# Performance work log

Measured on AMD Instinct MI355X. Metric: run time of the kernel, lower is better.

The kernel has to match this reference:

```python
import jax, jax.numpy as jnp
import numpy as np

EMBED = 4096
NUM_Q = 32
NUM_KV = 8
GROUPS = NUM_Q // NUM_KV  # 4
HEAD_DIM = EMBED // NUM_Q  # 128
KV_DIM = HEAD_DIM * NUM_KV  # 1024


def setup_inputs() -> dict:
    key = jax.random.key(0)
    ks = jax.random.split(key, 12)
    B, S = 2, 2048
    s = 0.02
    return {
        "query": jax.random.normal(ks[0], (B, S, EMBED), jnp.float32),
        "key": jax.random.normal(ks[1], (B, S, EMBED), jnp.float32),
        "value": jax.random.normal(ks[2], (B, S, EMBED), jnp.float32),
        # weights stored [in, out] (i.e. torch weight transposed)
        "Wq": jax.random.normal(ks[3], (EMBED, EMBED), jnp.float32) * s,
        "bq": jnp.zeros((EMBED,), jnp.float32),
        "Wk": jax.random.normal(ks[4], (EMBED, KV_DIM), jnp.float32) * s,
        "bk": jnp.zeros((KV_DIM,), jnp.float32),
        "Wv": jax.random.normal(ks[5], (EMBED, KV_DIM), jnp.float32) * s,
        "bv": jnp.zeros((KV_DIM,), jnp.float32),
        "Wo": jax.random.normal(ks[6], (EMBED, EMBED), jnp.float32) * s,
        "bo": jnp.zeros((EMBED,), jnp.float32),
    }


def reference(query, key, value, Wq, bq, Wk, bk, Wv, bv, Wo, bo):
    B, S, _ = query.shape
    Q = query @ Wq + bq                      # [B,S,E]
    K = key @ Wk + bk                        # [B,S,KV_DIM]
    V = value @ Wv + bv                      # [B,S,KV_DIM]
    # Q head h attends kv head h // GROUPS (repeat_interleave semantics):
    # reshape Q heads as (kv_head, group)
    Q = Q.reshape(B, S, NUM_KV, GROUPS, HEAD_DIM).transpose(0, 2, 3, 1, 4)  # [B,Hkv,G,S,D]
    K = K.reshape(B, S, NUM_KV, HEAD_DIM).transpose(0, 2, 1, 3)             # [B,Hkv,S,D]
    V = V.reshape(B, S, NUM_KV, HEAD_DIM).transpose(0, 2, 1, 3)             # [B,Hkv,S,D]
    scale = 1.0 / jnp.sqrt(jnp.asarray(HEAD_DIM, query.dtype))
    scores = jnp.einsum('bhgqd,bhkd->bhgqk', Q, K) * scale  # [B,Hkv,G,S,S]
    w = jax.nn.softmax(scores, axis=-1)
    y = jnp.einsum('bhgqk,bhkd->bhgqd', w, V)                # [B,Hkv,G,S,D]
    # back to [B,S,E] with head order (kv_head*GROUPS + group)
    y = y.transpose(0, 3, 1, 2, 4).reshape(B, S, EMBED)
    return y @ Wo + bo  # dropout is identity in eval mode
```

## Files before the change

kernel.cpp:

```cpp
#include <hip/hip_runtime.h>

typedef unsigned short u16;
typedef __attribute__((ext_vector_type(8))) short s16x8;
typedef __attribute__((ext_vector_type(4))) short s16x4;
typedef __attribute__((ext_vector_type(4))) float f32x4;

#define DEVI static __device__ __forceinline__

constexpr int BATCH = 2;
constexpr int SEQ   = 2048;
constexpr int EMB   = 4096;
constexpr int NQ    = 32;
constexpr int NKV   = 8;
constexpr int HD    = 128;
constexpr int KVD   = 1024;
constexpr int MR    = BATCH * SEQ;

constexpr float SCL = 0.08838834764831845f * 1.4426950408889634f;


DEVI u16 f2bf(float f) {
  union { float f; unsigned u; } x; x.f = f;
  unsigned r = x.u + 0x7FFFu + ((x.u >> 16) & 1u);
  return (u16)(r >> 16);
}

DEVI void mfma_acc(f32x4& c, s16x8 a, s16x8 b) {
  asm volatile("v_mfma_f32_16x16x32_bf16 %0, %1, %2, %0" : "+v"(c) : "v"(a), "v"(b));
}

DEVI void gload16(const void* g, void* l) {
  __builtin_amdgcn_global_load_lds(
      (const __attribute__((address_space(1))) void*)g,
      (__attribute__((address_space(3))) void*)l, 16, 0, 0);
}

DEVI float fexp2(float x) {
#if __has_builtin(__builtin_amdgcn_exp2f)
  return __builtin_amdgcn_exp2f(x);
#else
  return exp2f(x);
#endif
}

DEVI void store_out(u16* C, size_t idx, float v)   { C[idx] = f2bf(v); }
DEVI void store_out(float* C, size_t idx, float v) { C[idx] = v; }


__global__ __launch_bounds__(256) void prep(
    const float* __restrict__ q_in, const float* __restrict__ k_in,
    const float* __restrict__ v_in,
    u16* __restrict__ qb, u16* __restrict__ kb, u16* __restrict__ vb,
    const float* __restrict__ Wq, const float* __restrict__ Wo,
    const float* __restrict__ Wk, const float* __restrict__ Wv,
    u16* __restrict__ Tq, u16* __restrict__ To,
    u16* __restrict__ Tk, u16* __restrict__ Tv) {
  __shared__ u16 tile[32][33];
  const int tid = threadIdx.x;
  int id = blockIdx.x;

  if (id < 24576) {
    const int tn = id >> 13;
    const float* in = (tn == 0) ? q_in : (tn == 1) ? k_in : v_in;
    u16* out = (tn == 0) ? qb : (tn == 1) ? kb : vb;
    const size_t i = (size_t)(id & 8191) * 256 + tid;
    const float4* p4 = (const float4*)in;
    float4 x = p4[2 * i], y = p4[2 * i + 1];
    u16 t[8];
    t[0] = f2bf(x.x); t[1] = f2bf(x.y); t[2] = f2bf(x.z); t[3] = f2bf(x.w);
    t[4] = f2bf(y.x); t[5] = f2bf(y.y); t[6] = f2bf(y.z); t[7] = f2bf(y.w);
    *(s16x8*)(out + 8 * i) = *(const s16x8*)t;
    return;
  }

  id -= 24576;
  int z, rem;
  if (id < 16384)      { z = 0; rem = id; }
  else if (id < 32768) { z = 1; rem = id - 16384; }
  else if (id < 36864) { z = 2; rem = id - 32768; }
  else                 { z = 3; rem = id - 36864; }
  const int nt = (z < 2) ? 128 : 32;
  const int Nd = (z < 2) ? EMB : KVD;
  const int bx = rem % nt, by = rem / nt;
  const float* W = (z == 0) ? Wq : (z == 1) ? Wo : (z == 2) ? Wk : Wv;
  u16* Wt = (z == 0) ? Tq : (z == 1) ? To : (z == 2) ? Tk : Tv;
  const float s = (z == 0) ? SCL : 1.0f;
  const int tx = tid & 31, ty = tid >> 5;
  const int n0 = bx * 32, k0 = by * 32;
#pragma unroll
  for (int j = 0; j < 4; ++j)
    tile[ty + 8 * j][tx] = f2bf(W[(size_t)(k0 + ty + 8 * j) * Nd + n0 + tx] * s);
  __syncthreads();
#pragma unroll
  for (int j = 0; j < 4; ++j)
    Wt[(size_t)(n0 + ty + 8 * j) * EMB + k0 + tx] = tile[tx][ty + 8 * j];
}


template <typename OT, int MODE>
DEVI void gemm_body(const u16* __restrict__ A, const u16* __restrict__ Bt,
                    const float* __restrict__ bias, float bscl, OT* __restrict__ C,
                    int M, int N, int K, int m0, int n0,
                    u16* As, u16* Bs) {
  const int tid = threadIdx.x;
  const int lane = tid & 63, w = tid >> 6;
  const int wr = w >> 1, wc = w & 1;
  const int l15 = lane & 15, g = lane >> 4;
  const int srow = lane >> 3;
  const int schunk = lane & 7;

  f32x4 acc[4][4] = {};

  const u16* Ag = A  + (size_t)(m0 + w * 8 + srow) * K + ((schunk ^ srow) << 3);
  const u16* Bg = Bt + (size_t)(n0 + w * 8 + srow) * K + ((schunk ^ srow) << 3);
  u16* Al = As + w * 512;
  u16* Bl = Bs + w * 512;

  for (int k0 = 0; k0 < K; k0 += 64) {
    __syncthreads();
#pragma unroll
    for (int p = 0; p < 4; ++p) {
      gload16(Ag + (size_t)(p * 32) * K + k0, Al + p * 2048);
      gload16(Bg + (size_t)(p * 32) * K + k0, Bl + p * 2048);
    }
    __syncthreads();

#pragma unroll
    for (int ks = 0; ks < 2; ++ks) {
      s16x8 af[4], bfr[4];
#pragma unroll
      for (int rt = 0; rt < 4; ++rt) {
        const int blk = ((ks << 2) | g) ^ (l15 & 7);
        af[rt] = *(const s16x8*)(As + (wr * 64 + rt * 16 + l15) * 64 + (blk << 3));
      }
#pragma unroll
      for (int ct = 0; ct < 4; ++ct) {
        const int blk = ((ks << 2) | g) ^ (l15 & 7);
        bfr[ct] = *(const s16x8*)(Bs + (wc * 64 + ct * 16 + l15) * 64 + (blk << 3));
      }
#pragma unroll
      for (int rt = 0; rt < 4; ++rt)
#pragma unroll
        for (int ct = 0; ct < 4; ++ct)
          mfma_acc(acc[rt][ct], af[rt], bfr[ct]);
    }
  }

#pragma unroll
  for (int ct = 0; ct < 4; ++ct) {
    const int col = n0 + wc * 64 + ct * 16 + l15;
    const float bv = bias[col] * bscl;
#pragma unroll
    for (int rt = 0; rt < 4; ++rt) {
      const int row0 = m0 + wr * 64 + rt * 16 + g * 4;
      if constexpr (MODE == 0) {
#pragma unroll
        for (int i = 0; i < 4; ++i)
          store_out(C, (size_t)(row0 + i) * N + col, acc[rt][ct][i] + bv);
      } else {
        const int b = row0 >> 11, s0 = row0 & 2047;
        const int h = col >> 7, d = col & 127;
        u16 t4[4];
#pragma unroll
        for (int i = 0; i < 4; ++i) t4[i] = f2bf(acc[rt][ct][i] + bv);
        *(s16x4*)((u16*)C + ((size_t)(b * NKV + h) * HD + d) * SEQ + s0) =
            *(const s16x4*)t4;
      }
    }
  }
}

__global__ __launch_bounds__(256) void gemm_o(const u16* __restrict__ A,
                                              const u16* __restrict__ Bt,
                                              const float* __restrict__ bias,
                                              float* __restrict__ C) {
  __shared__ __align__(16) u16 As[128 * 64];
  __shared__ __align__(16) u16 Bs[128 * 64];
  const int d = blockIdx.x + blockIdx.y * 32;
  const int t = (d & 7) * 128 + (d >> 3);
  const int x = t >> 5, y = t & 31;
  gemm_body<float, 0>(A, Bt, bias, 1.0f, C, MR, EMB, EMB, y * 128, x * 128, As, Bs);
}

__global__ __launch_bounds__(256) void gemm_proj(
    const u16* __restrict__ qb, const u16* __restrict__ kb, const u16* __restrict__ vb,
    const u16* __restrict__ Wqt, const u16* __restrict__ Wkt, const u16* __restrict__ Wvt,
    const float* __restrict__ bq, const float* __restrict__ bk, const float* __restrict__ bv,
    u16* __restrict__ Qp, u16* __restrict__ Kpp, u16* __restrict__ Vtt) {
  __shared__ __align__(16) u16 As[128 * 64];
  __shared__ __align__(16) u16 Bs[128 * 64];
  const int d = blockIdx.x + blockIdx.y * 48;
  const int t = (d & 7) * 192 + (d >> 3);
  const int x = t >> 5, y = t & 31;
  if (x < 32)
    gemm_body<u16, 0>(qb, Wqt, bq, SCL, Qp, MR, EMB, EMB, y * 128, x * 128, As, Bs);
  else if (x < 40)
    gemm_body<u16, 0>(kb, Wkt, bk, 1.0f, Kpp, MR, KVD, EMB, y * 128, (x - 32) * 128, As, Bs);
  else
    gemm_body<u16, 1>(vb, Wvt, bv, 1.0f, Vtt, MR, KVD, EMB, y * 128, (x - 40) * 128, As, Bs);
}


__global__ __launch_bounds__(256, 2) void attn(const u16* __restrict__ Q,
                                               const u16* __restrict__ Kp,
                                               const u16* __restrict__ Vt,
                                               u16* __restrict__ Y) {
  __shared__ __align__(16) u16 Kb[2][64 * 128];
  __shared__ __align__(16) u16 Vb[2][128 * 64];

  const int tid = threadIdx.x, lane = tid & 63, w = tid >> 6;
  const int l15 = lane & 15, g = lane >> 4;
  const int d_ = blockIdx.x;
  const int t_ = (d_ & 7) * 128 + (d_ >> 3);
  const int bz = t_ >> 4, b = bz >> 5, qh = bz & 31, h = qh >> 2;
  const int q0 = (t_ & 15) * 128;

  s16x8 qf[2][4];
  const u16* qptr = Q + (size_t)(b * SEQ + q0 + w * 32) * EMB + qh * HD;
#pragma unroll
  for (int rt = 0; rt < 2; ++rt)
#pragma unroll
    for (int ks = 0; ks < 4; ++ks)
      qf[rt][ks] = *(const s16x8*)(qptr + (size_t)(rt * 16 + l15) * EMB + ks * 32 + g * 8);

  const u16* kbase = Kp + (size_t)b * SEQ * KVD + h * HD;
  const u16* vbase = Vt + (size_t)(b * NKV + h) * HD * SEQ;

  auto stage = [&](int buf, int kv0) {
#pragma unroll
    for (int p = 0; p < 4; ++p) {
      int r = p * 16 + w * 4 + (lane >> 4);
      const u16* src = kbase + (size_t)(kv0 + r) * KVD + (((lane & 15) ^ (r & 7)) << 3);
      gload16(src, &Kb[buf][p * 2048 + w * 512]);
    }
#pragma unroll
    for (int p = 0; p < 4; ++p) {
      int r = p * 32 + w * 8 + (lane >> 3);
      const u16* src = vbase + (size_t)r * SEQ + kv0 + (((lane & 7) ^ (r & 7)) << 3);
      gload16(src, &Vb[buf][p * 2048 + w * 512]);
    }
  };

  f32x4 o[2][8] = {};
  float m_[2] = {-1e30f, -1e30f}, l_[2] = {0.f, 0.f};

  stage(0, 0);
  __syncthreads();

  for (int t = 0; t < SEQ / 64; ++t) {
    const int cur = t & 1;
    if (t < SEQ / 64 - 1) stage(cur ^ 1, (t + 1) * 64);

    f32x4 sacc[2][4] = {};
    __builtin_amdgcn_s_setprio(1);
#pragma unroll
    for (int ks = 0; ks < 4; ++ks) {
      s16x8 kf[4];
#pragma unroll
      for (int ct = 0; ct < 4; ++ct) {
        const int blk = ((ks << 2) | g) ^ (l15 & 7);
        kf[ct] = *(const s16x8*)&Kb[cur][(ct * 16 + l15) * 128 + (blk << 3)];
      }
#pragma unroll
      for (int rt = 0; rt < 2; ++rt)
#pragma unroll
        for (int ct = 0; ct < 4; ++ct)
          mfma_acc(sacc[rt][ct], kf[ct], qf[rt][ks]);
    }
    __builtin_amdgcn_s_setprio(0);

    s16x8 pvf[2][2];
#pragma unroll
    for (int rt = 0; rt < 2; ++rt) {
      float t0 = fmaxf(fmaxf(sacc[rt][0][0], sacc[rt][0][1]),
                       fmaxf(sacc[rt][0][2], sacc[rt][0][3]));
      float t1 = fmaxf(fmaxf(sacc[rt][1][0], sacc[rt][1][1]),
                       fmaxf(sacc[rt][1][2], sacc[rt][1][3]));
      float t2 = fmaxf(fmaxf(sacc[rt][2][0], sacc[rt][2][1]),
                       fmaxf(sacc[rt][2][2], sacc[rt][2][3]));
      float t3 = fmaxf(fmaxf(sacc[rt][3][0], sacc[rt][3][1]),
                       fmaxf(sacc[rt][3][2], sacc[rt][3][3]));
      const float pm = fmaxf(fmaxf(t0, t1), fmaxf(t2, t3));

      if (!__all(pm - m_[rt] <= 8.f)) {
        float mr = pm;
        mr = fmaxf(mr, __shfl_xor(mr, 16));
        mr = fmaxf(mr, __shfl_xor(mr, 32));
        const float mn = fmaxf(m_[rt], mr);
        const float al = fexp2(m_[rt] - mn);
        m_[rt] = mn;
        l_[rt] *= al;
#pragma unroll
        for (int dt = 0; dt < 8; ++dt) {
          o[rt][dt][0] *= al; o[rt][dt][1] *= al;
          o[rt][dt][2] *= al; o[rt][dt][3] *= al;
        }
      }
      const float mcur = m_[rt];

      float rs = 0.f;
      int wd[4][2];
#pragma unroll
      for (int ct = 0; ct < 4; ++ct) {
        float p0 = fexp2(sacc[rt][ct][0] - mcur);
        float p1 = fexp2(sacc[rt][ct][1] - mcur);
        float p2 = fexp2(sacc[rt][ct][2] - mcur);
        float p3 = fexp2(sacc[rt][ct][3] - mcur);
        rs += (p0 + p1) + (p2 + p3);
        asm("v_cvt_pk_bf16_f32 %0, %1, %2" : "=v"(wd[ct][0]) : "v"(p0), "v"(p1));
        asm("v_cvt_pk_bf16_f32 %0, %1, %2" : "=v"(wd[ct][1]) : "v"(p2), "v"(p3));
      }
      l_[rt] += rs;

#pragma unroll
      for (int ks2 = 0; ks2 < 2; ++ks2) {
        union { int w4[4]; s16x8 v; } u;
#pragma unroll
        for (int s = 0; s < 2; ++s) {
          int x = wd[2 * ks2][s], y = wd[2 * ks2 + 1][s];
          asm volatile("v_permlane32_swap_b32 %0, %1" : "+v"(x), "+v"(y));
          asm volatile("v_permlane16_swap_b32 %0, %1" : "+v"(x), "+v"(y));
          u.w4[s] = x; u.w4[2 + s] = y;
        }
        pvf[rt][ks2] = u.v;
      }
    }

    __builtin_amdgcn_s_setprio(1);
#pragma unroll
    for (int ks2 = 0; ks2 < 2; ++ks2)
#pragma unroll
      for (int dt = 0; dt < 8; ++dt) {
        const int blk = ((ks2 << 2) | g) ^ (l15 & 7);
        const s16x8 vf = *(const s16x8*)&Vb[cur][(dt * 16 + l15) * 64 + (blk << 3)];
        mfma_acc(o[0][dt], vf, pvf[0][ks2]);
        mfma_acc(o[1][dt], vf, pvf[1][ks2]);
      }
    __builtin_amdgcn_s_setprio(0);

    __syncthreads();
  }

  u16* ybase = Y + (size_t)(b * SEQ + q0 + w * 32) * EMB + qh * HD;
#pragma unroll
  for (int rt = 0; rt < 2; ++rt) {
    float lt = l_[rt];
    lt += __shfl_xor(lt, 16);
    lt += __shfl_xor(lt, 32);
    const float inv = 1.f / lt;
    u16* yr = ybase + (size_t)(rt * 16 + l15) * EMB + g * 4;
#pragma unroll
    for (int dt = 0; dt < 8; ++dt) {
      u16 t4[4];
#pragma unroll
      for (int i = 0; i < 4; ++i) t4[i] = f2bf(o[rt][dt][i] * inv);
      *(s16x4*)(yr + dt * 16) = *(const s16x4*)t4;
    }
  }
}


extern "C" void kernel_launch(void* const* d_in, const int* in_sizes, int n_in,
                              void* d_out, int out_size, void* d_ws, size_t ws_size,
                              hipStream_t stream) {
  (void)in_sizes; (void)n_in; (void)out_size;
  const float* q_in = (const float*)d_in[0];
  const float* k_in = (const float*)d_in[1];
  const float* v_in = (const float*)d_in[2];
  const float* Wq = (const float*)d_in[3];
  const float* bq = (const float*)d_in[4];
  const float* Wk = (const float*)d_in[5];
  const float* bk = (const float*)d_in[6];
  const float* Wv = (const float*)d_in[7];
  const float* bv = (const float*)d_in[8];
  const float* Wo = (const float*)d_in[9];
  const float* bo = (const float*)d_in[10];
  float* out = (float*)d_out;

  char* base = (char*)d_ws;
  size_t off = 0;
  auto alloc = [&](size_t bytes) -> void* {
    void* r = base + off;
    off += (bytes + 255) & ~(size_t)255;
    return r;
  };
  u16* qb  = (u16*)alloc((size_t)MR * EMB * 2);
  u16* kb  = (u16*)alloc((size_t)MR * EMB * 2);
  u16* vb  = (u16*)alloc((size_t)MR * EMB * 2);
  u16* Wqt = (u16*)alloc((size_t)EMB * EMB * 2);
  u16* Wkt = (u16*)alloc((size_t)KVD * EMB * 2);
  u16* Wvt = (u16*)alloc((size_t)KVD * EMB * 2);
  u16* Wot = (u16*)alloc((size_t)EMB * EMB * 2);
  u16* Qp  = (u16*)alloc((size_t)MR * EMB * 2);
  u16* Kpp = (u16*)alloc((size_t)MR * KVD * 2);
  u16* Vtt = (u16*)alloc((size_t)MR * KVD * 2);
  u16* Y   = qb;
  if (off > ws_size) return;

  prep<<<65536, 256, 0, stream>>>(q_in, k_in, v_in, qb, kb, vb,
                                  Wq, Wo, Wk, Wv, Wqt, Wot, Wkt, Wvt);

  gemm_proj<<<dim3(48, 32), 256, 0, stream>>>(qb, kb, vb, Wqt, Wkt, Wvt,
                                              bq, bk, bv, Qp, Kpp, Vtt);
  attn<<<1024, 256, 0, stream>>>(Qp, Kpp, Vtt, Y);
  gemm_o<<<dim3(32, 32), 256, 0, stream>>>(Y, Wot, bo, out);
}
```

Baseline: 633.5 us.

## Double-buffer GEMM LDS tiles with K-step 32 and async prefetch

Restructures the shared GEMM body to use two LDS buffers with a K-step of 32 instead of a single buffer with K-step 64. The next tile's global-to-LDS loads are issued before computing on the current one, with explicit vmcnt waits and barriers. This is meant to hide global load latency behind MFMA work, and the LDS swizzle is changed to suit 32-wide rows. Each iteration now does half the MFMA work between two barriers, so barrier overhead per FLOP goes up.

```diff
diff --git a/kernel.cpp b/kernel.cpp
--- a/kernel.cpp
+++ b/kernel.cpp
@@ -106,44 +106,56 @@
   const int lane = tid & 63, w = tid >> 6;
   const int wr = w >> 1, wc = w & 1;
   const int l15 = lane & 15, g = lane >> 4;
-  const int srow = lane >> 3;
-  const int schunk = lane & 7;
+  const int srow = lane >> 2, schunk = lane & 3;
+  const int fsw = (srow ^ (srow >> 2)) & 3;
+  const int fr  = (l15  ^ (l15  >> 2)) & 3;
 
   f32x4 acc[4][4] = {};
 
-  const u16* Ag = A  + (size_t)(m0 + w * 8 + srow) * K + ((schunk ^ srow) << 3);
-  const u16* Bg = Bt + (size_t)(n0 + w * 8 + srow) * K + ((schunk ^ srow) << 3);
-  u16* Al = As + w * 512;
-  u16* Bl = Bs + w * 512;
-
-  for (int k0 = 0; k0 < K; k0 += 64) {
-    __syncthreads();
-#pragma unroll
-    for (int p = 0; p < 4; ++p) {
-      gload16(Ag + (size_t)(p * 32) * K + k0, Al + p * 2048);
-      gload16(Bg + (size_t)(p * 32) * K + k0, Bl + p * 2048);
-    }
-    __syncthreads();
-
-#pragma unroll
-    for (int ks = 0; ks < 2; ++ks) {
-      s16x8 af[4], bfr[4];
-#pragma unroll
-      for (int rt = 0; rt < 4; ++rt) {
-        const int blk = ((ks << 2) | g) ^ (l15 & 7);
-        af[rt] = *(const s16x8*)(As + (wr * 64 + rt * 16 + l15) * 64 + (blk << 3));
-      }
-#pragma unroll
-      for (int ct = 0; ct < 4; ++ct) {
-        const int blk = ((ks << 2) | g) ^ (l15 & 7);
-        bfr[ct] = *(const s16x8*)(Bs + (wc * 64 + ct * 16 + l15) * 64 + (blk << 3));
-      }
-#pragma unroll
-      for (int rt = 0; rt < 4; ++rt)
-#pragma unroll
-        for (int ct = 0; ct < 4; ++ct)
-          mfma_acc(acc[rt][ct], af[rt], bfr[ct]);
-    }
+  const u16* Ag = A  + (size_t)(m0 + w * 32 + srow) * K + ((schunk ^ fsw) << 3);
+  const u16* Bg = Bt + (size_t)(n0 + w * 32 + srow) * K + ((schunk ^ fsw) << 3);
+
+  auto stage = [&](int buf, int k0) {
+    u16* Al = As + buf * 4096 + w * 1024;
+    u16* Bl = Bs + buf * 4096 + w * 1024;
+    gload16(Ag + k0,                    Al);
+    gload16(Ag + (size_t)16 * K + k0,   Al + 16 * 32);
+    gload16(Bg + k0,                    Bl);
+    gload16(Bg + (size_t)16 * K + k0,   Bl + 16 * 32);
+  };
+
+  stage(0, 0);
+  const int ns = K >> 5;
+  for (int s = 0; s < ns; ++s) {
+    const int cur = s & 1;
+    if (s + 1 < ns) {
+      stage(cur ^ 1, (s + 1) << 5);
+      asm volatile("s_waitcnt vmcnt(4)" ::: "memory");
+    } else {
+      asm volatile("s_waitcnt vmcnt(0)" ::: "memory");
+    }
+    __builtin_amdgcn_sched_barrier(0);
+    __builtin_amdgcn_s_barrier();
+    __builtin_amdgcn_sched_barrier(0);
+
+    const u16* Ab = As + cur * 4096;
+    const u16* Bb = Bs + cur * 4096;
+    s16x8 af[4], bfr[4];
+#pragma unroll
+    for (int rt = 0; rt < 4; ++rt)
+      af[rt] = *(const s16x8*)(Ab + (wr * 64 + rt * 16 + l15) * 32 + ((g ^ fr) << 3));
+#pragma unroll
+    for (int ct = 0; ct < 4; ++ct)
+      bfr[ct] = *(const s16x8*)(Bb + (wc * 64 + ct * 16 + l15) * 32 + ((g ^ fr) << 3));
+#pragma unroll
+    for (int rt = 0; rt < 4; ++rt)
+#pragma unroll
+      for (int ct = 0; ct < 4; ++ct)
+        mfma_acc(acc[rt][ct], af[rt], bfr[ct]);
+
+    __builtin_amdgcn_sched_barrier(0);
+    __builtin_amdgcn_s_barrier();
+    __builtin_amdgcn_sched_barrier(0);
   }
 
 #pragma unroll
@@ -174,8 +186,8 @@
                                               const u16* __restrict__ Bt,
                                               const float* __restrict__ bias,
                                               float* __restrict__ C) {
-  __shared__ __align__(16) u16 As[128 * 64];
-  __shared__ __align__(16) u16 Bs[128 * 64];
+  __shared__ __align__(16) u16 As[2 * 128 * 32];
+  __shared__ __align__(16) u16 Bs[2 * 128 * 32];
   const int d = blockIdx.x + blockIdx.y * 32;
   const int t = (d & 7) * 128 + (d >> 3);
   const int x = t >> 5, y = t & 31;
@@ -187,8 +199,8 @@
     const u16* __restrict__ Wqt, const u16* __restrict__ Wkt, const u16* __restrict__ Wvt,
     const float* __restrict__ bq, const float* __restrict__ bk, const float* __restrict__ bv,
     u16* __restrict__ Qp, u16* __restrict__ Kpp, u16* __restrict__ Vtt) {
-  __shared__ __align__(16) u16 As[128 * 64];
-  __shared__ __align__(16) u16 Bs[128 * 64];
+  __shared__ __align__(16) u16 As[2 * 128 * 32];
+  __shared__ __align__(16) u16 Bs[2 * 128 * 32];
   const int d = blockIdx.x + blockIdx.y * 48;
   const int t = (d & 7) * 192 + (d >> 3);
   const int x = t >> 5, y = t & 31;
```

Measured after the change: 684.1 us. 1.08x slower.

## Double-buffer LDS tiles in projection GEMMs to overlap global loads with MFMA

Applied to the files above, without the earlier changes.

Doubles the shared-memory A/B tile buffers in the shared GEMM body and prefetches the next K-slice into the alternate buffer while the current one is consumed by MFMAs. Partial vmcnt waits plus explicit barriers around sched_barriers replace the two full syncthreads per iteration. This targets global-to-LDS load latency stalls in the QKV and output projections, at the cost of doubled LDS per block (64KB), which may reduce occupancy.

```diff
diff --git a/kernel.cpp b/kernel.cpp
--- a/kernel.cpp
+++ b/kernel.cpp
@@ -113,30 +113,45 @@
 
   const u16* Ag = A  + (size_t)(m0 + w * 8 + srow) * K + ((schunk ^ srow) << 3);
   const u16* Bg = Bt + (size_t)(n0 + w * 8 + srow) * K + ((schunk ^ srow) << 3);
-  u16* Al = As + w * 512;
-  u16* Bl = Bs + w * 512;
-
-  for (int k0 = 0; k0 < K; k0 += 64) {
-    __syncthreads();
+
+  auto stage = [&](int buf, int k0) {
+    u16* Al = As + buf * 8192 + w * 512;
+    u16* Bl = Bs + buf * 8192 + w * 512;
 #pragma unroll
     for (int p = 0; p < 4; ++p) {
       gload16(Ag + (size_t)(p * 32) * K + k0, Al + p * 2048);
       gload16(Bg + (size_t)(p * 32) * K + k0, Bl + p * 2048);
     }
-    __syncthreads();
-
+  };
+
+  stage(0, 0);
+  const int ns = K >> 6;
+  for (int s = 0; s < ns; ++s) {
+    const int cur = s & 1;
+    if (s + 1 < ns) {
+      stage(cur ^ 1, (s + 1) << 6);
+      asm volatile("s_waitcnt vmcnt(8)" ::: "memory");
+    } else {
+      asm volatile("s_waitcnt vmcnt(0)" ::: "memory");
+    }
+    __builtin_amdgcn_sched_barrier(0);
+    __builtin_amdgcn_s_barrier();
+    __builtin_amdgcn_sched_barrier(0);
+
+    const u16* Ab = As + cur * 8192;
+    const u16* Bb = Bs + cur * 8192;
 #pragma unroll
     for (int ks = 0; ks < 2; ++ks) {
       s16x8 af[4], bfr[4];
 #pragma unroll
       for (int rt = 0; rt < 4; ++rt) {
         const int blk = ((ks << 2) | g) ^ (l15 & 7);
-        af[rt] = *(const s16x8*)(As + (wr * 64 + rt * 16 + l15) * 64 + (blk << 3));
+        af[rt] = *(const s16x8*)(Ab + (wr * 64 + rt * 16 + l15) * 64 + (blk << 3));
       }
 #pragma unroll
       for (int ct = 0; ct < 4; ++ct) {
         const int blk = ((ks << 2) | g) ^ (l15 & 7);
-        bfr[ct] = *(const s16x8*)(Bs + (wc * 64 + ct * 16 + l15) * 64 + (blk << 3));
+        bfr[ct] = *(const s16x8*)(Bb + (wc * 64 + ct * 16 + l15) * 64 + (blk << 3));
       }
 #pragma unroll
       for (int rt = 0; rt < 4; ++rt)
@@ -144,6 +159,10 @@
         for (int ct = 0; ct < 4; ++ct)
           mfma_acc(acc[rt][ct], af[rt], bfr[ct]);
     }
+
+    __builtin_amdgcn_sched_barrier(0);
+    __builtin_amdgcn_s_barrier();
+    __builtin_amdgcn_sched_barrier(0);
   }
 
 #pragma unroll
@@ -174,8 +193,8 @@
                                               const u16* __restrict__ Bt,
                                               const float* __restrict__ bias,
                                               float* __restrict__ C) {
-  __shared__ __align__(16) u16 As[128 * 64];
-  __shared__ __align__(16) u16 Bs[128 * 64];
+  __shared__ __align__(16) u16 As[2 * 128 * 64];
+  __shared__ __align__(16) u16 Bs[2 * 128 * 64];
   const int d = blockIdx.x + blockIdx.y * 32;
   const int t = (d & 7) * 128 + (d >> 3);
   const int x = t >> 5, y = t & 31;
@@ -187,8 +206,8 @@
     const u16* __restrict__ Wqt, const u16* __restrict__ Wkt, const u16* __restrict__ Wvt,
     const float* __restrict__ bq, const float* __restrict__ bk, const float* __restrict__ bv,
     u16* __restrict__ Qp, u16* __restrict__ Kpp, u16* __restrict__ Vtt) {
-  __shared__ __align__(16) u16 As[128 * 64];
-  __shared__ __align__(16) u16 Bs[128 * 64];
+  __shared__ __align__(16) u16 As[2 * 128 * 64];
+  __shared__ __align__(16) u16 Bs[2 * 128 * 64];
   const int d = blockIdx.x + blockIdx.y * 48;
   const int t = (d & 7) * 192 + (d >> 3);
   const int x = t >> 5, y = t & 31;
```

Measured after the change: 714.8 us. 12.8% more time.
